# Optimization experiments

Hardware: AMD Instinct MI355X
Metric: run time of the kernel (lower is better)

The kernel has to match this reference:

```python
import jax, jax.numpy as jnp
import numpy as np

INPUT, HIDDEN, OUTPUT = 512, 1024, 512

def setup_inputs() -> dict:
    key = jax.random.key(0)
    ks = jax.random.split(key, 6)
    s_i = 1.0 / np.sqrt(INPUT)
    s_h = 1.0 / np.sqrt(HIDDEN)
    return {
        "x": jax.random.normal(ks[0], (64, 512, INPUT), dtype=jnp.float32),
        "Wi": jax.random.normal(ks[1], (INPUT, HIDDEN), dtype=jnp.float32) * s_i,
        "bi": jax.random.normal(ks[2], (HIDDEN,), dtype=jnp.float32) * 0.01,
        "Wh": jax.random.normal(ks[3], (HIDDEN, HIDDEN), dtype=jnp.float32) * s_h,
        "Wo": jax.random.normal(ks[4], (HIDDEN, OUTPUT), dtype=jnp.float32) * s_h,
        "bo": jax.random.normal(ks[5], (OUTPUT,), dtype=jnp.float32) * 0.01,
    }

def reference(x, Wi, bi, Wh, Wo, bo):
    B, S, _ = x.shape
    # Precompute input projection for all timesteps: [B,S,H]
    xi = jnp.einsum("bsi,ih->bsh", x, Wi) + bi
    h0 = jnp.zeros((B, Wh.shape[0]), dtype=x.dtype)

    def scan_fn(h, xi_t):
        # flax SimpleCell: tanh(dense_i(x) + dense_h(h)); module applies relu on top
        h_next = jax.nn.relu(jnp.tanh(xi_t + h @ Wh))
        return h_next, h_next

    _, h_stacked = jax.lax.scan(scan_fn, h0, jnp.transpose(xi, (1, 0, 2)))  # [S,B,H]
    h_stacked = jnp.transpose(h_stacked, (1, 0, 2))  # [B,S,H]
    y = jnp.einsum("bsh,ho->bso", h_stacked, Wo) + bo
    return y
```

## Files before the change

### kernel.cpp

```cpp
#include <hip/hip_runtime.h>
#include <math.h>

#define BATCH   64
#define SEQ     512
#define NIN     512
#define NHID    1024
#define NOUT    512

typedef short short8 __attribute__((ext_vector_type(8)));
typedef float f32x4 __attribute__((ext_vector_type(4)));

__device__ __forceinline__ unsigned short f2bf(float f) {
  unsigned int u = __float_as_uint(f);
  unsigned int r = (u + 0x7fffu + ((u >> 16) & 1u)) >> 16;
  return (unsigned short)r;
}

#define BM 128
#define BN 64
#define BK 16

__global__ __launch_bounds__(256) void gemm_bias(
    const float* __restrict__ A, const float* __restrict__ B,
    const float* __restrict__ bias, float* __restrict__ C,
    int M, int N, int K) {
  __shared__ float As[BK][BM + 4];
  __shared__ float Bs[BK][BN + 4];

  const int tid = threadIdx.x;
  const int bx = blockIdx.x;
  const int by = blockIdx.y;

  const int tm = (tid / 16) * 8;
  const int tn = (tid % 16) * 4;

  const int ar = tid / 4;
  const int ac = (tid % 4) * 4;
  const int br = tid / 16;
  const int bc = (tid % 16) * 4;

  float acc[8][4] = {};

  for (int k0 = 0; k0 < K; k0 += BK) {
    float4 av0 = *(const float4*)&A[(size_t)(by * BM + ar) * K + k0 + ac];
    float4 av1 = *(const float4*)&A[(size_t)(by * BM + ar + 64) * K + k0 + ac];
    As[ac + 0][ar] = av0.x;  As[ac + 0][ar + 64] = av1.x;
    As[ac + 1][ar] = av0.y;  As[ac + 1][ar + 64] = av1.y;
    As[ac + 2][ar] = av0.z;  As[ac + 2][ar + 64] = av1.z;
    As[ac + 3][ar] = av0.w;  As[ac + 3][ar + 64] = av1.w;
    float4 bv = *(const float4*)&B[(size_t)(k0 + br) * N + bx * BN + bc];
    *(float4*)&Bs[br][bc] = bv;
    __syncthreads();

#pragma unroll
    for (int k = 0; k < BK; ++k) {
      float4 a0 = *(const float4*)&As[k][tm];
      float4 a1 = *(const float4*)&As[k][tm + 4];
      float4 b4 = *(const float4*)&Bs[k][tn];
      float ae[8] = {a0.x, a0.y, a0.z, a0.w, a1.x, a1.y, a1.z, a1.w};
      float be[4] = {b4.x, b4.y, b4.z, b4.w};
#pragma unroll
      for (int i = 0; i < 8; ++i)
#pragma unroll
        for (int j = 0; j < 4; ++j)
          acc[i][j] = fmaf(ae[i], be[j], acc[i][j]);
    }
    __syncthreads();
  }

  const float4 bb = *(const float4*)&bias[bx * BN + tn];
#pragma unroll
  for (int i = 0; i < 8; ++i) {
    float4 o;
    o.x = acc[i][0] + bb.x;
    o.y = acc[i][1] + bb.y;
    o.z = acc[i][2] + bb.z;
    o.w = acc[i][3] + bb.w;
    *(float4*)&C[(size_t)(by * BM + tm + i) * N + bx * BN + tn] = o;
  }
}

#define OBM 128
#define OBN 128
#define OBK 32
#define LDK 40

__global__ __launch_bounds__(256) void gemm_bias_bf16(
    const float* __restrict__ A, const float* __restrict__ B,
    const float* __restrict__ bias, float* __restrict__ C,
    int M, int N, int K) {
  __shared__ unsigned short Asb[OBM][LDK];
  __shared__ unsigned short Bsb[OBN][LDK];

  const int tid  = threadIdx.x;
  const int lane = tid & 63;
  const int wid  = tid >> 6;
  const int wm   = wid >> 1;
  const int wn   = wid & 1;
  const int bx   = blockIdx.x;
  const int by   = blockIdx.y;

  const int ar  = tid >> 1;
  const int aks = (tid & 1) * 16;
  const int bk4 = (tid >> 5) * 4;
  const int bn4 = (tid & 31) * 4;

  const int l15 = lane & 15;
  const int lk8 = (lane >> 4) * 8;

  f32x4 acc[4][4];
#pragma unroll
  for (int i = 0; i < 4; ++i)
#pragma unroll
    for (int j = 0; j < 4; ++j) acc[i][j] = (f32x4){0.f, 0.f, 0.f, 0.f};

  for (int k0 = 0; k0 < K; k0 += OBK) {
    const float* Ap = &A[(size_t)(by * OBM + ar) * K + k0 + aks];
    float4 a0 = *(const float4*)(Ap + 0);
    float4 a1 = *(const float4*)(Ap + 4);
    float4 a2 = *(const float4*)(Ap + 8);
    float4 a3 = *(const float4*)(Ap + 12);
    unsigned short ta[16] = {
        f2bf(a0.x), f2bf(a0.y), f2bf(a0.z), f2bf(a0.w),
        f2bf(a1.x), f2bf(a1.y), f2bf(a1.z), f2bf(a1.w),
        f2bf(a2.x), f2bf(a2.y), f2bf(a2.z), f2bf(a2.w),
        f2bf(a3.x), f2bf(a3.y), f2bf(a3.z), f2bf(a3.w)};
    *(short8*)&Asb[ar][aks + 0] = *(short8*)&ta[0];
    *(short8*)&Asb[ar][aks + 8] = *(short8*)&ta[8];

#pragma unroll
    for (int kk = 0; kk < 4; ++kk) {
      float4 bv = *(const float4*)&B[(size_t)(k0 + bk4 + kk) * N + bx * OBN + bn4];
      Bsb[bn4 + 0][bk4 + kk] = f2bf(bv.x);
      Bsb[bn4 + 1][bk4 + kk] = f2bf(bv.y);
      Bsb[bn4 + 2][bk4 + kk] = f2bf(bv.z);
      Bsb[bn4 + 3][bk4 + kk] = f2bf(bv.w);
    }
    __syncthreads();

    short8 afr[4], bfr[4];
#pragma unroll
    for (int t = 0; t < 4; ++t) {
      afr[t] = *(const short8*)&Asb[wm * 64 + t * 16 + l15][lk8];
      bfr[t] = *(const short8*)&Bsb[wn * 64 + t * 16 + l15][lk8];
    }
#pragma unroll
    for (int rt = 0; rt < 4; ++rt)
#pragma unroll
      for (int ct = 0; ct < 4; ++ct)
        acc[rt][ct] = __builtin_amdgcn_mfma_f32_16x16x32_bf16(
            afr[rt], bfr[ct], acc[rt][ct], 0, 0, 0);
    __syncthreads();
  }

#pragma unroll
  for (int rt = 0; rt < 4; ++rt) {
    const int row0 = by * OBM + wm * 64 + rt * 16 + (lane >> 4) * 4;
#pragma unroll
    for (int ct = 0; ct < 4; ++ct) {
      const int col = bx * OBN + wn * 64 + ct * 16 + l15;
      const float bb = bias[col];
#pragma unroll
      for (int i = 0; i < 4; ++i)
        C[(size_t)(row0 + i) * N + col] = acc[rt][ct][i] + bb;
    }
  }
}

#define GROUPS 8
#define BPG    32
#define BPERG  8

#define FMA4(hv, wv4, accv)              \
  accv.x = fmaf(hv, wv4.x, accv.x);      \
  accv.y = fmaf(hv, wv4.y, accv.y);      \
  accv.z = fmaf(hv, wv4.z, accv.z);      \
  accv.w = fmaf(hv, wv4.w, accv.w);

__global__ __launch_bounds__(256, 1) void rnn_scan_ws(
    const float* __restrict__ Wh, float* __restrict__ xi,
    unsigned int* flags) {
  __shared__ float hs[BPERG * NHID];
  __shared__ float P[256 * 32];

  const int tid  = threadIdx.x;
  const int bg   = blockIdx.x & 7;
  const int jc   = blockIdx.x >> 3;
  const int c4   = tid & 7;
  const int kseg = tid >> 3;
  const int colbase = jc * 32 + c4 * 4;
  const int hswz  = (kseg & 7) << 2;
  const int stswz = ((tid >> 3) & 7) << 2;
  const int ob   = tid >> 5;
  const int ocol = tid & 31;
  const int oc4  = ocol >> 2;
  const int oce  = ocol & 3;

  float4 w[32];
#pragma unroll
  for (int kk = 0; kk < 32; ++kk)
    w[kk] = *(const float4*)&Wh[(size_t)(kseg * 32 + kk) * NHID + colbase];

  float* const xrow_base =
      xi + (size_t)(bg * BPERG + ob) * SEQ * NHID + jc * 32 + ocol;
  unsigned int* const gflags = flags + bg * 32;
  unsigned int* const myflag = gflags + jc;
  unsigned int* const pollflag = gflags + (tid & 31);

  float xin = __hip_atomic_load(xrow_base, __ATOMIC_RELAXED,
                                __HIP_MEMORY_SCOPE_AGENT);

  for (int s = 0; s < SEQ; ++s) {
    float* prow = xrow_base + (size_t)s * NHID;

    float4 acc[BPERG];
#pragma unroll
    for (int b = 0; b < BPERG; ++b) acc[b] = make_float4(0.f, 0.f, 0.f, 0.f);

    if (s > 0) {
      const float* base =
          xi + (size_t)(bg * BPERG) * SEQ * NHID + (size_t)(s - 1) * NHID + tid * 4;
#pragma unroll
      for (int b = 0; b < BPERG; ++b) {
        float4 v = *(const float4*)(base + (size_t)b * SEQ * NHID);
        *(float4*)&hs[b * NHID + ((tid * 4) ^ stswz)] = v;
      }
      __syncthreads();

#pragma unroll
      for (int b = 0; b < BPERG; ++b) {
#pragma unroll
        for (int kq = 0; kq < 8; ++kq) {
          const float4 h4 =
              *(const float4*)&hs[b * NHID + kseg * 32 + ((kq * 4) ^ hswz)];
          FMA4(h4.x, w[kq * 4 + 0], acc[b]);
          FMA4(h4.y, w[kq * 4 + 1], acc[b]);
          FMA4(h4.z, w[kq * 4 + 2], acc[b]);
          FMA4(h4.w, w[kq * 4 + 3], acc[b]);
        }
      }
    }

    {
      const int u = kseg * 8 + c4;
      const int sw = (((kseg & 7) ^ c4)) << 2;
#pragma unroll
      for (int b = 0; b < BPERG; ++b)
        *(float4*)&P[u * 32 + ((b * 4) ^ sw)] = acc[b];
    }
    __syncthreads();

    float sum = 0.f;
#pragma unroll
    for (int q = 0; q < 32; ++q) {
      const int uu = q * 8 + oc4;
      const int sw2 = ((q & 7) ^ oc4) << 2;
      sum += P[uu * 32 + ((ob * 4 + oce) ^ sw2)];
    }

    const float hn = fmaxf(tanhf(xin + sum), 0.f);
    __hip_atomic_store(prow, hn, __ATOMIC_RELAXED, __HIP_MEMORY_SCOPE_AGENT);

    __syncthreads();
    const unsigned int target = (unsigned int)(s + 1);
    if (tid == 0)
      __hip_atomic_store(myflag, target, __ATOMIC_RELAXED,
                         __HIP_MEMORY_SCOPE_AGENT);

    if (s + 1 < SEQ)
      xin = __hip_atomic_load(xrow_base + (size_t)(s + 1) * NHID,
                              __ATOMIC_RELAXED, __HIP_MEMORY_SCOPE_AGENT);

    if (tid < 64) {
      while (true) {
        unsigned int v = __hip_atomic_load(pollflag, __ATOMIC_RELAXED,
                                           __HIP_MEMORY_SCOPE_AGENT);
        if (__all(v >= target)) break;
        __builtin_amdgcn_s_sleep(1);
      }
    }
    __syncthreads();
  }
}

extern "C" void kernel_launch(void* const* d_in, const int* in_sizes, int n_in,
                              void* d_out, int out_size, void* d_ws, size_t ws_size,
                              hipStream_t stream) {
  const float* x  = (const float*)d_in[0];
  const float* Wi = (const float*)d_in[1];
  const float* bi = (const float*)d_in[2];
  const float* Wh = (const float*)d_in[3];
  const float* Wo = (const float*)d_in[4];
  const float* bo = (const float*)d_in[5];
  float* out = (float*)d_out;
  float* xi  = (float*)d_ws;

  unsigned int* flags = (unsigned int*)d_out;

  const int M = BATCH * SEQ;

  dim3 blk(256);
  hipMemsetAsync(flags, 0, GROUPS * BPG * sizeof(unsigned int), stream);
  gemm_bias<<<dim3(NHID / BN, M / BM), blk, 0, stream>>>(x, Wi, bi, xi, M, NHID, NIN);
  {
    const float* Wh_p = Wh;
    float* xi_p = xi;
    unsigned int* flags_p = flags;
    void* args[3] = {(void*)&Wh_p, (void*)&xi_p, (void*)&flags_p};
    hipLaunchCooperativeKernel((const void*)rnn_scan_ws, dim3(GROUPS * BPG),
                               dim3(256), args, 0, stream);
  }
  gemm_bias_bf16<<<dim3(NOUT / OBN, M / OBM), blk, 0, stream>>>(xi, Wo, bo, out,
                                                               M, NOUT, NHID);
}
```

Baseline: 2.481 ms.

## Add fast L2-coherent flag sync with timeout fallback to system-coherent backup path

```diff
diff --git a/kernel.cpp b/kernel.cpp
--- a/kernel.cpp
+++ b/kernel.cpp
@@ -9,6 +9,7 @@
 
 typedef short short8 __attribute__((ext_vector_type(8)));
 typedef float f32x4 __attribute__((ext_vector_type(4)));
+typedef float f32x4v __attribute__((ext_vector_type(4)));
 
 __device__ __forceinline__ unsigned short f2bf(float f) {
   unsigned int u = __float_as_uint(f);
@@ -170,12 +171,21 @@
 #define GROUPS 8
 #define BPG    32
 #define BPERG  8
+#define POLL_BOUND 16384
 
 #define FMA4(hv, wv4, accv)              \
   accv.x = fmaf(hv, wv4.x, accv.x);      \
   accv.y = fmaf(hv, wv4.y, accv.y);      \
   accv.z = fmaf(hv, wv4.z, accv.z);      \
   accv.w = fmaf(hv, wv4.w, accv.w);
+
+__device__ __forceinline__ float load_sc0_f32(const float* p) {
+  float v;
+  asm volatile("global_load_dword %0, %1, off sc0\n\ts_waitcnt vmcnt(0)"
+               : "=v"(v) : "v"(p) : "memory");
+  __builtin_amdgcn_sched_barrier(0);
+  return v;
+}
 
 __global__ __launch_bounds__(256, 1) void rnn_scan_ws(
     const float* __restrict__ Wh, float* __restrict__ xi,
@@ -203,27 +213,52 @@
 
   float* const xrow_base =
       xi + (size_t)(bg * BPERG + ob) * SEQ * NHID + jc * 32 + ocol;
-  unsigned int* const gflags = flags + bg * 32;
-  unsigned int* const myflag = gflags + jc;
-  unsigned int* const pollflag = gflags + (tid & 31);
-
-  float xin = __hip_atomic_load(xrow_base, __ATOMIC_RELAXED,
-                                __HIP_MEMORY_SCOPE_AGENT);
+  unsigned int* const fastflags = flags;
+  unsigned int* const slowflags = flags + 256;
+  float* const backup = (float*)(flags + 512);
+  unsigned int* const myfast = fastflags + bg * 32 + jc;
+  unsigned int* const myslow = slowflags + bg * 32 + jc;
+  const unsigned int* const pollfast = fastflags + bg * 32 + (tid & 31);
+  const unsigned int* const pollslow = slowflags + bg * 32 + (tid & 31);
+
+  const int bk_row_self = bg * BPERG + ob;
+  const int bk_col_self = jc * 32 + ocol;
+
+  bool sticky_slow = false;
+
+  float xin = load_sc0_f32(xrow_base);
 
   for (int s = 0; s < SEQ; ++s) {
-    float* prow = xrow_base + (size_t)s * NHID;
-
     float4 acc[BPERG];
 #pragma unroll
     for (int b = 0; b < BPERG; ++b) acc[b] = make_float4(0.f, 0.f, 0.f, 0.f);
 
     if (s > 0) {
-      const float* base =
-          xi + (size_t)(bg * BPERG) * SEQ * NHID + (size_t)(s - 1) * NHID + tid * 4;
-#pragma unroll
-      for (int b = 0; b < BPERG; ++b) {
-        float4 v = *(const float4*)(base + (size_t)b * SEQ * NHID);
-        *(float4*)&hs[b * NHID + ((tid * 4) ^ stswz)] = v;
+      if (!sticky_slow) {
+        const float* base = xi + (size_t)(bg * BPERG) * SEQ * NHID +
+                            (size_t)(s - 1) * NHID + tid * 4;
+#pragma unroll
+        for (int b = 0; b < BPERG; ++b) {
+          float4 v = *(const float4*)(base + (size_t)b * SEQ * NHID);
+          *(float4*)&hs[b * NHID + ((tid * 4) ^ stswz)] = v;
+        }
+      } else {
+        const float* bb = backup + ((size_t)((s - 1) & 1) * 64) * 1024 +
+                          (size_t)(bg * BPERG) * 1024 + tid * 4;
+        f32x4v bv[BPERG];
+#pragma unroll
+        for (int b = 0; b < BPERG; ++b) {
+          asm volatile("global_load_dwordx4 %0, %1, off sc0 sc1"
+                       : "=v"(bv[b]) : "v"(bb + (size_t)b * 1024) : "memory");
+        }
+        asm volatile("s_waitcnt vmcnt(0)" ::: "memory");
+        __builtin_amdgcn_sched_barrier(0);
+#pragma unroll
+        for (int b = 0; b < BPERG; ++b) {
+          float4 v;
+          v.x = bv[b][0]; v.y = bv[b][1]; v.z = bv[b][2]; v.w = bv[b][3];
+          *(float4*)&hs[b * NHID + ((tid * 4) ^ stswz)] = v;
+        }
       }
       __syncthreads();
 
@@ -259,24 +294,63 @@
     }
 
     const float hn = fmaxf(tanhf(xin + sum), 0.f);
-    __hip_atomic_store(prow, hn, __ATOMIC_RELAXED, __HIP_MEMORY_SCOPE_AGENT);
+    xi[(size_t)bk_row_self * SEQ * NHID + (size_t)s * NHID + bk_col_self] = hn;
+    hs[tid] = hn;
 
     __syncthreads();
     const unsigned int target = (unsigned int)(s + 1);
+    if (tid == 0) *myfast = target;
+
+    {
+      float* const bslot = backup + (size_t)(s & 1) * 64 * 1024;
+      if (tid >= 64) {
+        __hip_atomic_store(
+            bslot + (size_t)bk_row_self * 1024 + bk_col_self, hn,
+            __ATOMIC_RELAXED, __HIP_MEMORY_SCOPE_AGENT);
+        if (tid < 128) {
+          const int u = tid - 64;
+          __hip_atomic_store(
+              bslot + (size_t)(bg * BPERG + (u >> 5)) * 1024 + jc * 32 +
+                  (u & 31),
+              hs[u], __ATOMIC_RELAXED, __HIP_MEMORY_SCOPE_AGENT);
+        }
+      }
+    }
+
+    if (s + 1 < SEQ)
+      xin = load_sc0_f32(xrow_base + (size_t)(s + 1) * NHID);
+
+    bool timedout = false;
+    if (!sticky_slow) {
+      if (tid < 64) {
+        int it = 0;
+        while (true) {
+          unsigned int v;
+          asm volatile("global_load_dword %0, %1, off sc0\n\ts_waitcnt vmcnt(0)"
+                       : "=v"(v) : "v"(pollfast) : "memory");
+          __builtin_amdgcn_sched_barrier(0);
+          if (__all(v >= target)) break;
+          if (++it >= POLL_BOUND) { timedout = true; break; }
+          __builtin_amdgcn_s_sleep(1);
+        }
+      }
+      if (__syncthreads_or((tid < 64) && timedout)) sticky_slow = true;
+      else continue;
+    }
+
+    __syncthreads();
     if (tid == 0)
-      __hip_atomic_store(myflag, target, __ATOMIC_RELAXED,
+      __hip_atomic_store(myslow, target, __ATOMIC_RELAXED,
                          __HIP_MEMORY_SCOPE_AGENT);
-
-    if (s + 1 < SEQ)
-      xin = __hip_atomic_load(xrow_base + (size_t)(s + 1) * NHID,
-                              __ATOMIC_RELAXED, __HIP_MEMORY_SCOPE_AGENT);
-
     if (tid < 64) {
       while (true) {
-        unsigned int v = __hip_atomic_load(pollflag, __ATOMIC_RELAXED,
-                                           __HIP_MEMORY_SCOPE_AGENT);
+        unsigned int v;
+        asm volatile(
+            "global_load_dword %0, %1, off sc0 sc1\n\ts_waitcnt vmcnt(0)"
+            : "=v"(v) : "v"(pollslow) : "memory");
+        __builtin_amdgcn_sched_barrier(0);
         if (__all(v >= target)) break;
-        __builtin_amdgcn_s_sleep(1);
+        __builtin_amdgcn_s_sleep(8);
       }
     }
     __syncthreads();
@@ -300,7 +374,7 @@
   const int M = BATCH * SEQ;
 
   dim3 blk(256);
-  hipMemsetAsync(flags, 0, GROUPS * BPG * sizeof(unsigned int), stream);
+  hipMemsetAsync(flags, 0, 2048 + 2 * 64 * 1024 * sizeof(float), stream);
   gemm_bias<<<dim3(NHID / BN, M / BM), blk, 0, stream>>>(x, Wi, bi, xi, M, NHID, NIN);
   {
     const float* Wh_p = Wh;
```

After: 4.252 ms. +71.4%, slower.

## Fuse input projection GEMM into cooperative RNN scan kernel with producer blocks

Applied to the files above, without the earlier changes.

```diff
diff --git a/kernel.cpp b/kernel.cpp
--- a/kernel.cpp
+++ b/kernel.cpp
@@ -15,6 +15,16 @@
   unsigned int r = (u + 0x7fffu + ((u >> 16) & 1u)) >> 16;
   return (unsigned short)r;
 }
+
+#define GROUPS 8
+#define BPG    32
+#define BPERG  8
+
+#define FMA4(hv, wv4, accv)              \
+  accv.x = fmaf(hv, wv4.x, accv.x);      \
+  accv.y = fmaf(hv, wv4.y, accv.y);      \
+  accv.z = fmaf(hv, wv4.z, accv.z);      \
+  accv.w = fmaf(hv, wv4.w, accv.w);
 
 #define BM 128
 #define BN 64
@@ -167,16 +177,6 @@
   }
 }
 
-#define GROUPS 8
-#define BPG    32
-#define BPERG  8
-
-#define FMA4(hv, wv4, accv)              \
-  accv.x = fmaf(hv, wv4.x, accv.x);      \
-  accv.y = fmaf(hv, wv4.y, accv.y);      \
-  accv.z = fmaf(hv, wv4.z, accv.z);      \
-  accv.w = fmaf(hv, wv4.w, accv.w);
-
 __global__ __launch_bounds__(256, 1) void rnn_scan_ws(
     const float* __restrict__ Wh, float* __restrict__ xi,
     unsigned int* flags) {
@@ -283,6 +283,196 @@
   }
 }
 
+__global__ __launch_bounds__(256, 2) void rnn_fused(
+    const float* __restrict__ Wh, const float* __restrict__ Wi,
+    const float* __restrict__ x, const float* __restrict__ bi,
+    float* __restrict__ xi, unsigned int* flags) {
+  __shared__ float smem[16384];
+  const int tid = threadIdx.x;
+  unsigned int* const xi_done = flags + 256;
+
+  if (blockIdx.x >= GROUPS * BPG) {
+    const int bw = blockIdx.x - GROUPS * BPG;
+    float* As = smem;
+    float* Bs = smem + 16 * 132;
+    const int tm = (tid / 16) * 8;
+    const int tn = (tid % 16) * 4;
+    const int ar = tid / 4;
+    const int ac = (tid % 4) * 4;
+    const int br = tid / 16;
+    const int bc = (tid % 16) * 4;
+    const int b0 = ar >> 1;
+    const int so = ar & 1;
+
+    for (int i = 0; i < 16; ++i) {
+      const int j = (i << 8) + bw;
+      const int st = j >> 4;
+      const int ct = j & 15;
+      const int s2 = 2 * st + so;
+
+      float acc[8][4] = {};
+      for (int k0 = 0; k0 < NIN; k0 += 16) {
+        float4 av0 = *(const float4*)&x[((size_t)b0 * SEQ + s2) * NIN + k0 + ac];
+        float4 av1 =
+            *(const float4*)&x[((size_t)(b0 + 32) * SEQ + s2) * NIN + k0 + ac];
+        As[(ac + 0) * 132 + ar] = av0.x;  As[(ac + 0) * 132 + ar + 64] = av1.x;
+        As[(ac + 1) * 132 + ar] = av0.y;  As[(ac + 1) * 132 + ar + 64] = av1.y;
+        As[(ac + 2) * 132 + ar] = av0.z;  As[(ac + 2) * 132 + ar + 64] = av1.z;
+        As[(ac + 3) * 132 + ar] = av0.w;  As[(ac + 3) * 132 + ar + 64] = av1.w;
+        float4 bv = *(const float4*)&Wi[(size_t)(k0 + br) * NHID + ct * 64 + bc];
+        *(float4*)&Bs[br * 68 + bc] = bv;
+        __syncthreads();
+
+#pragma unroll
+        for (int k = 0; k < 16; ++k) {
+          float4 a0 = *(const float4*)&As[k * 132 + tm];
+          float4 a1 = *(const float4*)&As[k * 132 + tm + 4];
+          float4 b4 = *(const float4*)&Bs[k * 68 + tn];
+          float ae[8] = {a0.x, a0.y, a0.z, a0.w, a1.x, a1.y, a1.z, a1.w};
+          float be[4] = {b4.x, b4.y, b4.z, b4.w};
+#pragma unroll
+          for (int ii = 0; ii < 8; ++ii)
+#pragma unroll
+            for (int jj = 0; jj < 4; ++jj)
+              acc[ii][jj] = fmaf(ae[ii], be[jj], acc[ii][jj]);
+        }
+        __syncthreads();
+      }
+
+      const float4 bb = *(const float4*)&bi[ct * 64 + tn];
+#pragma unroll
+      for (int r = 0; r < 8; ++r) {
+        const int row = tm + r;
+        const int b = row >> 1;
+        const int s = 2 * st + (row & 1);
+        f32x4 o;
+        o[0] = acc[r][0] + bb.x;
+        o[1] = acc[r][1] + bb.y;
+        o[2] = acc[r][2] + bb.z;
+        o[3] = acc[r][3] + bb.w;
+        float* cp = xi + ((size_t)b * SEQ + s) * NHID + ct * 64 + tn;
+        asm volatile("global_store_dwordx4 %0, %1, off sc0 sc1"
+                     :: "v"(cp), "v"(o) : "memory");
+      }
+      asm volatile("s_waitcnt vmcnt(0)" ::: "memory");
+      __builtin_amdgcn_sched_barrier(0);
+      __syncthreads();
+      if (tid == 0) atomicAdd(&xi_done[st], 1u);
+      __syncthreads();
+    }
+    return;
+  }
+
+  __builtin_amdgcn_s_setprio(1);
+  float* hs = smem;
+  float* P  = smem + 8192;
+
+  const int bg   = blockIdx.x & 7;
+  const int jc   = blockIdx.x >> 3;
+  const int c4   = tid & 7;
+  const int kseg = tid >> 3;
+  const int colbase = jc * 32 + c4 * 4;
+  const int hswz  = (kseg & 7) << 2;
+  const int stswz = ((tid >> 3) & 7) << 2;
+  const int ob   = tid >> 5;
+  const int ocol = tid & 31;
+  const int oc4  = ocol >> 2;
+  const int oce  = ocol & 3;
+
+  float4 w[32];
+#pragma unroll
+  for (int kk = 0; kk < 32; ++kk)
+    w[kk] = *(const float4*)&Wh[(size_t)(kseg * 32 + kk) * NHID + colbase];
+
+  float* const xrow_base =
+      xi + (size_t)(bg * BPERG + ob) * SEQ * NHID + jc * 32 + ocol;
+  unsigned int* const gflags = flags + bg * 32;
+  unsigned int* const myflag = gflags + jc;
+
+  if (tid < 64) {
+    while (__hip_atomic_load(xi_done, __ATOMIC_RELAXED,
+                             __HIP_MEMORY_SCOPE_AGENT) < 16u)
+      __builtin_amdgcn_s_sleep(1);
+  }
+  __syncthreads();
+
+  for (int s = 0; s < SEQ; ++s) {
+    float* prow = xrow_base + (size_t)s * NHID;
+    const float xin = __hip_atomic_load(prow, __ATOMIC_RELAXED,
+                                        __HIP_MEMORY_SCOPE_AGENT);
+
+    float4 acc[BPERG];
+#pragma unroll
+    for (int b = 0; b < BPERG; ++b) acc[b] = make_float4(0.f, 0.f, 0.f, 0.f);
+
+    if (s > 0) {
+      const float* base =
+          xi + (size_t)(bg * BPERG) * SEQ * NHID + (size_t)(s - 1) * NHID + tid * 4;
+#pragma unroll
+      for (int b = 0; b < BPERG; ++b) {
+        float4 v = *(const float4*)(base + (size_t)b * SEQ * NHID);
+        *(float4*)&hs[b * NHID + ((tid * 4) ^ stswz)] = v;
+      }
+      __syncthreads();
+
+#pragma unroll
+      for (int b = 0; b < BPERG; ++b) {
+#pragma unroll
+        for (int kq = 0; kq < 8; ++kq) {
+          const float4 h4 =
+              *(const float4*)&hs[b * NHID + kseg * 32 + ((kq * 4) ^ hswz)];
+          FMA4(h4.x, w[kq * 4 + 0], acc[b]);
+          FMA4(h4.y, w[kq * 4 + 1], acc[b]);
+          FMA4(h4.z, w[kq * 4 + 2], acc[b]);
+          FMA4(h4.w, w[kq * 4 + 3], acc[b]);
+        }
+      }
+    }
+
+    {
+      const int u = kseg * 8 + c4;
+      const int sw = (((kseg & 7) ^ c4)) << 2;
+#pragma unroll
+      for (int b = 0; b < BPERG; ++b)
+        *(float4*)&P[u * 32 + ((b * 4) ^ sw)] = acc[b];
+    }
+    __syncthreads();
+
+    float sum = 0.f;
+#pragma unroll
+    for (int q = 0; q < 32; ++q) {
+      const int uu = q * 8 + oc4;
+      const int sw2 = ((q & 7) ^ oc4) << 2;
+      sum += P[uu * 32 + ((ob * 4 + oce) ^ sw2)];
+    }
+
+    const float hn = fmaxf(tanhf(xin + sum), 0.f);
+    __hip_atomic_store(prow, hn, __ATOMIC_RELAXED, __HIP_MEMORY_SCOPE_AGENT);
+
+    __syncthreads();
+    const unsigned int target = (unsigned int)(s + 1);
+    if (tid == 0)
+      __hip_atomic_store(myflag, target, __ATOMIC_RELAXED,
+                         __HIP_MEMORY_SCOPE_AGENT);
+
+    if (tid < 64) {
+      const int nxt = s + 1;
+      const int tile = (nxt < SEQ) ? (nxt >> 1) : 0;
+      const unsigned int thr =
+          (tid < 32) ? target : ((nxt < SEQ) ? 16u : 0u);
+      const unsigned int* pp =
+          (tid < 32) ? (gflags + tid) : (xi_done + tile);
+      while (true) {
+        unsigned int v = __hip_atomic_load(pp, __ATOMIC_RELAXED,
+                                           __HIP_MEMORY_SCOPE_AGENT);
+        if (__all(v >= thr)) break;
+        __builtin_amdgcn_s_sleep(1);
+      }
+    }
+    __syncthreads();
+  }
+}
+
 extern "C" void kernel_launch(void* const* d_in, const int* in_sizes, int n_in,
                               void* d_out, int out_size, void* d_ws, size_t ws_size,
                               hipStream_t stream) {
@@ -300,9 +490,31 @@
   const int M = BATCH * SEQ;
 
   dim3 blk(256);
-  hipMemsetAsync(flags, 0, GROUPS * BPG * sizeof(unsigned int), stream);
-  gemm_bias<<<dim3(NHID / BN, M / BM), blk, 0, stream>>>(x, Wi, bi, xi, M, NHID, NIN);
-  {
+  hipMemsetAsync(flags, 0, 2048, stream);
+
+  int occ = 0;
+  hipError_t qerr = hipOccupancyMaxActiveBlocksPerMultiprocessor(
+      &occ, (const void*)rnn_fused, 256, 0);
+  bool fused_ok = (qerr == hipSuccess) && (occ >= 2);
+
+  if (fused_ok) {
+    const float* Wh_p = Wh;
+    const float* Wi_p = Wi;
+    const float* x_p  = x;
+    const float* bi_p = bi;
+    float* xi_p = xi;
+    unsigned int* flags_p = flags;
+    void* args[6] = {(void*)&Wh_p, (void*)&Wi_p, (void*)&x_p,
+                     (void*)&bi_p, (void*)&xi_p, (void*)&flags_p};
+    hipError_t err = hipLaunchCooperativeKernel(
+        (const void*)rnn_fused, dim3(GROUPS * BPG + 256), dim3(256), args, 0,
+        stream);
+    fused_ok = (err == hipSuccess);
+  }
+
+  if (!fused_ok) {
+    gemm_bias<<<dim3(NHID / BN, M / BM), blk, 0, stream>>>(x, Wi, bi, xi, M,
+                                                           NHID, NIN);
     const float* Wh_p = Wh;
     float* xi_p = xi;
     unsigned int* flags_p = flags;
@@ -310,6 +522,7 @@
     hipLaunchCooperativeKernel((const void*)rnn_scan_ws, dim3(GROUPS * BPG),
                                dim3(256), args, 0, stream);
   }
+
   gemm_bias_bf16<<<dim3(NOUT / OBN, M / OBM), blk, 0, stream>>>(xi, Wo, bo, out,
                                                                M, NOUT, NHID);
 }
```

Result: no change. 2.467 ms (-0.6%).
